# Optimization experiments

Hardware: AMD Instinct MI355X
Metric: run time of the kernel (lower is better)

Reference implementation:

```python
import jax, jax.numpy as jnp
import numpy as np

B = 65536            # batch of configurations
F = 32               # num_frames (joints)
DOF = 29             # controllable joints
# tree: chain 0..29, two mimic branches off frame 10; parent index always < child -> topo order = range(F)
PARENTS = [-1] + list(range(29)) + [10, 10]


def _np_rodrigues(w):
    th = np.linalg.norm(w)
    if th < 1e-12:
        return np.eye(3)
    k = w / th
    K = np.array([[0, -k[2], k[1]], [k[2], 0, -k[0]], [-k[1], k[0], 0]])
    return np.eye(3) + np.sin(th) * K + (1 - np.cos(th)) * (K @ K)


def setup_inputs() -> dict:
    key = jax.random.key(0)
    rng = np.random.default_rng(0)
    # joint types: 0 fixed, 1 revolute, 2 prismatic
    types = np.ones(F, dtype=np.int32)
    types[0] = 0
    types[15] = 2
    types[22] = 2
    # controllable = non-fixed, non-mimic (mimic dst = 30, 31)
    ctrl = np.array([i for i in range(F) if types[i] != 0 and i not in (30, 31)], dtype=np.int32)
    assert ctrl.shape[0] == DOF
    axes = rng.normal(size=(F, 3)).astype(np.float32)
    axes /= np.linalg.norm(axes, axis=-1, keepdims=True)
    origins = np.tile(np.eye(4, dtype=np.float32), (F, 1, 1))
    for i in range(F):
        origins[i, :3, :3] = _np_rodrigues(rng.normal(size=3) * 0.5)
        origins[i, :3, 3] = rng.normal(size=3) * 0.1
    joint_angles = jax.random.normal(key, (B, DOF), dtype=jnp.float32)
    return {
        "joint_angles": joint_angles,
        "all_axes": jnp.asarray(axes),
        "all_origins": jnp.asarray(origins),
        "mimic_multipliers": jnp.array([1.0, -1.0], dtype=jnp.float32),
        "mimic_offsets": jnp.array([0.1, -0.1], dtype=jnp.float32),
        "ctrlable_indices": jnp.asarray(ctrl),
        "mimic_src_indices": jnp.array([5, 6], dtype=jnp.int32),
        "mimic_dst_indices": jnp.array([30, 31], dtype=jnp.int32),
        "joint_types": jnp.asarray(types),
    }


def exp_map(w):
    # axis-angle (...,3) -> rotation (...,3,3), Rodrigues, eps-safe at w=0
    theta = jnp.sqrt(jnp.sum(w * w, axis=-1, keepdims=True) + 1e-18)  # (...,1)
    k = w / theta
    kx, ky, kz = k[..., 0], k[..., 1], k[..., 2]
    zero = jnp.zeros_like(kx)
    K = jnp.stack(
        [jnp.stack([zero, -kz, ky], -1),
         jnp.stack([kz, zero, -kx], -1),
         jnp.stack([-ky, kx, zero], -1)], -2)
    st = jnp.sin(theta)[..., None]
    ct = jnp.cos(theta)[..., None]
    return jnp.eye(3, dtype=w.dtype) + st * K + (1.0 - ct) * (K @ K)


def _fk(joint_angles, all_axes, all_origins, mimic_multipliers, mimic_offsets,
        ctrlable_indices, mimic_src_indices, mimic_dst_indices, joint_types):
    b = joint_angles.shape[0]
    # scatter controllable angles, then mimic gather/scatter
    all_angles = jnp.zeros((b, F), joint_angles.dtype).at[:, ctrlable_indices].set(joint_angles)
    mimic_vals = all_angles[:, mimic_src_indices] * mimic_multipliers + mimic_offsets
    all_angles = all_angles.at[:, mimic_dst_indices].set(mimic_vals)
    # per-frame local motion (B,F,4,4)
    w = all_axes[None, :, :] * all_angles[..., None]          # (B,F,3)
    R = exp_map(w)                                            # (B,F,3,3)
    R = jnp.where((joint_types == 1)[None, :, None, None], R, jnp.eye(3, dtype=w.dtype))
    t = jnp.where((joint_types == 2)[None, :, None], w, jnp.zeros((), w.dtype))
    top = jnp.concatenate([R, t[..., None]], axis=-1)         # (B,F,3,4)
    bottom = jnp.broadcast_to(jnp.array([0, 0, 0, 1], w.dtype), (b, F, 1, 4))
    motion = jnp.concatenate([top, bottom], axis=-2)          # (B,F,4,4)
    local = jnp.einsum('fij,bfjk->bfik', all_origins, motion)
    # sequential tree-structured compose (F is small & static -> unrolled)
    poses = []
    for i in range(F):
        p = PARENTS[i]
        li = local[:, i]
        poses.append(li if p < 0 else poses[p] @ li)
    return jnp.stack(poses, axis=1)                            # (B,F,4,4)


def reference(joint_angles, all_axes, all_origins, mimic_multipliers, mimic_offsets,
              ctrlable_indices, mimic_src_indices, mimic_dst_indices, joint_types):
    return _fk(joint_angles, all_axes, all_origins, mimic_multipliers, mimic_offsets,
               ctrlable_indices, mimic_src_indices, mimic_dst_indices, joint_types)
```

## Files before the change

kernel.cpp:

```cpp
#include <hip/hip_runtime.h>
#include <math.h>

#define BLOCK 256
#define NF 32
#define NDOF 29

__global__ __launch_bounds__(BLOCK) void fk_kernel(
    const float* __restrict__ ja,
    const float* __restrict__ axes,
    const float* __restrict__ origins,
    const float* __restrict__ mmul,
    const float* __restrict__ moff,
    const int*   __restrict__ ctrl,
    const int*   __restrict__ msrc,
    const int*   __restrict__ mdst,
    const int*   __restrict__ types,
    float*       __restrict__ out,
    int B)
{
    __shared__ float s_ax[NF][3];
    __shared__ float s_or[NF][12];
    __shared__ int   s_type[NF];
    __shared__ int   s_slot[NF];
    __shared__ float s_mult[NF];
    __shared__ float s_off[NF];
    __shared__ float s_ja[BLOCK * NDOF];

    const int tid = threadIdx.x;

    if (tid < NF) {
        const int f = tid;
        s_ax[f][0] = axes[f*3+0];
        s_ax[f][1] = axes[f*3+1];
        s_ax[f][2] = axes[f*3+2];
        #pragma unroll
        for (int r = 0; r < 3; ++r)
            #pragma unroll
            for (int c = 0; c < 4; ++c)
                s_or[f][r*4+c] = origins[f*16 + r*4 + c];
        s_type[f] = types[f];
        int slot = -1;
        for (int j = 0; j < NDOF; ++j) if (ctrl[j] == f) slot = j;
        float mu = 1.0f, of = 0.0f;
        for (int m = 0; m < 2; ++m) {
            if (mdst[m] == f) {
                const int sf = msrc[m];
                for (int j = 0; j < NDOF; ++j) if (ctrl[j] == sf) slot = j;
                mu = mmul[m]; of = moff[m];
            }
        }
        s_slot[f] = slot; s_mult[f] = mu; s_off[f] = of;
    }

    const long blk0 = (long)blockIdx.x * BLOCK;
    {
        const long base = blk0 * NDOF;
        const long lim  = (long)B * NDOF;
        for (int i = tid; i < BLOCK * NDOF; i += BLOCK) {
            const long g = base + i;
            s_ja[i] = (g < lim) ? ja[g] : 0.0f;
        }
    }
    __syncthreads();

    const long b = blk0 + tid;
    if (b >= B) return;

    float4* __restrict__ outp = (float4*)(out + b * 512);

    float Pr[9], Pt[3];
    float Qr[9], Qt[3];

    auto compute_local = [&](int f, float* Lr, float* Lt) {
        const int   slot = s_slot[f];
        const float a = (slot >= 0) ? fmaf(s_mult[f], s_ja[tid*NDOF + slot], s_off[f]) : 0.0f;
        const float wx = a * s_ax[f][0];
        const float wy = a * s_ax[f][1];
        const float wz = a * s_ax[f][2];
        const int ty = s_type[f];
        float R0,R1,R2,R3,R4,R5,R6,R7,R8;
        if (ty == 1) {
            const float t2 = wx*wx + wy*wy + wz*wz;
            const float th = sqrtf(t2 + 1e-18f);
            const float inv = 1.0f / th;
            const float kx = wx*inv, ky = wy*inv, kz = wz*inv;
            float s, c;
            __sincosf(th, &s, &c);
            const float v = 1.0f - c;
            R0 = fmaf(v*kx, kx, c);
            R1 = v*kx*ky - s*kz;
            R2 = v*kx*kz + s*ky;
            R3 = v*kx*ky + s*kz;
            R4 = fmaf(v*ky, ky, c);
            R5 = v*ky*kz - s*kx;
            R6 = v*kx*kz - s*ky;
            R7 = v*ky*kz + s*kx;
            R8 = fmaf(v*kz, kz, c);
        } else {
            R0=1.f;R1=0.f;R2=0.f;R3=0.f;R4=1.f;R5=0.f;R6=0.f;R7=0.f;R8=1.f;
        }
        float tx, tyv, tz;
        if (ty == 2) { tx = wx; tyv = wy; tz = wz; }
        else         { tx = 0.f; tyv = 0.f; tz = 0.f; }
        const float* O = s_or[f];
        #pragma unroll
        for (int r = 0; r < 3; ++r) {
            const float o0 = O[r*4+0], o1 = O[r*4+1], o2 = O[r*4+2], o3 = O[r*4+3];
            Lr[r*3+0] = o0*R0 + o1*R3 + o2*R6;
            Lr[r*3+1] = o0*R1 + o1*R4 + o2*R7;
            Lr[r*3+2] = o0*R2 + o1*R5 + o2*R8;
            Lt[r]     = o0*tx + o1*tyv + o2*tz + o3;
        }
    };

    auto store_pose = [&](int f, const float* r, const float* t) {
        outp[f*4+0] = make_float4(r[0], r[1], r[2], t[0]);
        outp[f*4+1] = make_float4(r[3], r[4], r[5], t[1]);
        outp[f*4+2] = make_float4(r[6], r[7], r[8], t[2]);
        outp[f*4+3] = make_float4(0.0f, 0.0f, 0.0f, 1.0f);
    };

    {
        float Lr[9], Lt[3];
        compute_local(0, Lr, Lt);
        #pragma unroll
        for (int i = 0; i < 9; ++i) Pr[i] = Lr[i];
        Pt[0] = Lt[0]; Pt[1] = Lt[1]; Pt[2] = Lt[2];
        store_pose(0, Pr, Pt);
    }

    #pragma unroll 1
    for (int f = 1; f <= 29; ++f) {
        float Lr[9], Lt[3], Nr[9], Nt[3];
        compute_local(f, Lr, Lt);
        #pragma unroll
        for (int r = 0; r < 3; ++r) {
            const float p0 = Pr[r*3+0], p1 = Pr[r*3+1], p2 = Pr[r*3+2];
            Nr[r*3+0] = p0*Lr[0] + p1*Lr[3] + p2*Lr[6];
            Nr[r*3+1] = p0*Lr[1] + p1*Lr[4] + p2*Lr[7];
            Nr[r*3+2] = p0*Lr[2] + p1*Lr[5] + p2*Lr[8];
            Nt[r]     = p0*Lt[0] + p1*Lt[1] + p2*Lt[2] + Pt[r];
        }
        #pragma unroll
        for (int i = 0; i < 9; ++i) Pr[i] = Nr[i];
        Pt[0] = Nt[0]; Pt[1] = Nt[1]; Pt[2] = Nt[2];
        store_pose(f, Pr, Pt);
        if (f == 10) {
            #pragma unroll
            for (int i = 0; i < 9; ++i) Qr[i] = Pr[i];
            Qt[0] = Pt[0]; Qt[1] = Pt[1]; Qt[2] = Pt[2];
        }
    }

    #pragma unroll 1
    for (int f = 30; f < 32; ++f) {
        float Lr[9], Lt[3], Nr[9], Nt[3];
        compute_local(f, Lr, Lt);
        #pragma unroll
        for (int r = 0; r < 3; ++r) {
            const float p0 = Qr[r*3+0], p1 = Qr[r*3+1], p2 = Qr[r*3+2];
            Nr[r*3+0] = p0*Lr[0] + p1*Lr[3] + p2*Lr[6];
            Nr[r*3+1] = p0*Lr[1] + p1*Lr[4] + p2*Lr[7];
            Nr[r*3+2] = p0*Lr[2] + p1*Lr[5] + p2*Lr[8];
            Nt[r]     = p0*Lt[0] + p1*Lt[1] + p2*Lt[2] + Qt[r];
        }
        store_pose(f, Nr, Nt);
    }
}

extern "C" void kernel_launch(void* const* d_in, const int* in_sizes, int n_in,
                              void* d_out, int out_size, void* d_ws, size_t ws_size,
                              hipStream_t stream) {
    const float* ja   = (const float*)d_in[0];
    const float* axes = (const float*)d_in[1];
    const float* orig = (const float*)d_in[2];
    const float* mmul = (const float*)d_in[3];
    const float* moff = (const float*)d_in[4];
    const int*   ctrl = (const int*)d_in[5];
    const int*   msrc = (const int*)d_in[6];
    const int*   mdst = (const int*)d_in[7];
    const int*   typs = (const int*)d_in[8];
    float* out = (float*)d_out;

    const int B = in_sizes[0] / NDOF;
    const int grid = (B + BLOCK - 1) / BLOCK;
    fk_kernel<<<grid, BLOCK, 0, stream>>>(ja, axes, orig, mmul, moff,
                                          ctrl, msrc, mdst, typs, out, B);
}
```

Measured before the change: 183.9 us.

## Stage output poses through LDS for coalesced stores and transpose angle buffer

Joint angles are now stored in shared memory transposed with a padded stride, so each thread's per-joint read avoids bank conflicts. Output poses are computed two frames at a time into a padded shared staging buffer and then written cooperatively, so consecutive threads store consecutive 128-byte chunks instead of each thread striding 2 KB apart. This is meant to make the dominant 128 MB output write coalesced. In exchange it adds 32 block-wide barriers, about 37 KB more LDS per block, which may lower occupancy, and a single loop that branches on frame index.

```diff
diff --git a/kernel.cpp b/kernel.cpp
--- a/kernel.cpp
+++ b/kernel.cpp
@@ -4,6 +4,8 @@
 #define BLOCK 256
 #define NF 32
 #define NDOF 29
+#define ANG_STRIDE 257
+#define OUT_STRIDE_F4 9
 
 __global__ __launch_bounds__(BLOCK) void fk_kernel(
     const float* __restrict__ ja,
@@ -24,7 +26,8 @@
     __shared__ int   s_slot[NF];
     __shared__ float s_mult[NF];
     __shared__ float s_off[NF];
-    __shared__ float s_ja[BLOCK * NDOF];
+    __shared__ float s_ang[NDOF * ANG_STRIDE];
+    __shared__ float4 s_out[BLOCK * OUT_STRIDE_F4];
 
     const int tid = threadIdx.x;
 
@@ -58,22 +61,20 @@
         const long lim  = (long)B * NDOF;
         for (int i = tid; i < BLOCK * NDOF; i += BLOCK) {
             const long g = base + i;
-            s_ja[i] = (g < lim) ? ja[g] : 0.0f;
+            const int slot = i % NDOF;
+            const int brel = i / NDOF;
+            s_ang[slot * ANG_STRIDE + brel] = (g < lim) ? ja[g] : 0.0f;
         }
     }
     __syncthreads();
-
-    const long b = blk0 + tid;
-    if (b >= B) return;
-
-    float4* __restrict__ outp = (float4*)(out + b * 512);
 
     float Pr[9], Pt[3];
     float Qr[9], Qt[3];
 
     auto compute_local = [&](int f, float* Lr, float* Lt) {
         const int   slot = s_slot[f];
-        const float a = (slot >= 0) ? fmaf(s_mult[f], s_ja[tid*NDOF + slot], s_off[f]) : 0.0f;
+        const float a = (slot >= 0)
+            ? fmaf(s_mult[f], s_ang[slot * ANG_STRIDE + tid], s_off[f]) : 0.0f;
         const float wx = a * s_ax[f][0];
         const float wy = a * s_ax[f][1];
         const float wz = a * s_ax[f][2];
@@ -113,58 +114,67 @@
         }
     };
 
-    auto store_pose = [&](int f, const float* r, const float* t) {
-        outp[f*4+0] = make_float4(r[0], r[1], r[2], t[0]);
-        outp[f*4+1] = make_float4(r[3], r[4], r[5], t[1]);
-        outp[f*4+2] = make_float4(r[6], r[7], r[8], t[2]);
-        outp[f*4+3] = make_float4(0.0f, 0.0f, 0.0f, 1.0f);
-    };
-
-    {
-        float Lr[9], Lt[3];
-        compute_local(0, Lr, Lt);
-        #pragma unroll
-        for (int i = 0; i < 9; ++i) Pr[i] = Lr[i];
-        Pt[0] = Lt[0]; Pt[1] = Lt[1]; Pt[2] = Lt[2];
-        store_pose(0, Pr, Pt);
-    }
+    float4* const out4 = (float4*)out;
 
     #pragma unroll 1
-    for (int f = 1; f <= 29; ++f) {
-        float Lr[9], Lt[3], Nr[9], Nt[3];
-        compute_local(f, Lr, Lt);
+    for (int c = 0; c < 16; ++c) {
+        const int f0 = 2 * c;
         #pragma unroll
-        for (int r = 0; r < 3; ++r) {
-            const float p0 = Pr[r*3+0], p1 = Pr[r*3+1], p2 = Pr[r*3+2];
-            Nr[r*3+0] = p0*Lr[0] + p1*Lr[3] + p2*Lr[6];
-            Nr[r*3+1] = p0*Lr[1] + p1*Lr[4] + p2*Lr[7];
-            Nr[r*3+2] = p0*Lr[2] + p1*Lr[5] + p2*Lr[8];
-            Nt[r]     = p0*Lt[0] + p1*Lt[1] + p2*Lt[2] + Pt[r];
+        for (int lf = 0; lf < 2; ++lf) {
+            const int f = f0 + lf;
+            float Lr[9], Lt[3];
+            compute_local(f, Lr, Lt);
+            float Wr[9], Wt[3];
+            if (f == 0) {
+                #pragma unroll
+                for (int i = 0; i < 9; ++i) Wr[i] = Lr[i];
+                Wt[0]=Lt[0]; Wt[1]=Lt[1]; Wt[2]=Lt[2];
+            } else if (f <= 29) {
+                #pragma unroll
+                for (int r = 0; r < 3; ++r) {
+                    const float p0 = Pr[r*3+0], p1 = Pr[r*3+1], p2 = Pr[r*3+2];
+                    Wr[r*3+0] = p0*Lr[0] + p1*Lr[3] + p2*Lr[6];
+                    Wr[r*3+1] = p0*Lr[1] + p1*Lr[4] + p2*Lr[7];
+                    Wr[r*3+2] = p0*Lr[2] + p1*Lr[5] + p2*Lr[8];
+                    Wt[r]     = p0*Lt[0] + p1*Lt[1] + p2*Lt[2] + Pt[r];
+                }
+            } else {
+                #pragma unroll
+                for (int r = 0; r < 3; ++r) {
+                    const float p0 = Qr[r*3+0], p1 = Qr[r*3+1], p2 = Qr[r*3+2];
+                    Wr[r*3+0] = p0*Lr[0] + p1*Lr[3] + p2*Lr[6];
+                    Wr[r*3+1] = p0*Lr[1] + p1*Lr[4] + p2*Lr[7];
+                    Wr[r*3+2] = p0*Lr[2] + p1*Lr[5] + p2*Lr[8];
+                    Wt[r]     = p0*Lt[0] + p1*Lt[1] + p2*Lt[2] + Qt[r];
+                }
+            }
+            if (f <= 29) {
+                #pragma unroll
+                for (int i = 0; i < 9; ++i) Pr[i] = Wr[i];
+                Pt[0]=Wt[0]; Pt[1]=Wt[1]; Pt[2]=Wt[2];
+                if (f == 10) {
+                    #pragma unroll
+                    for (int i = 0; i < 9; ++i) Qr[i] = Pr[i];
+                    Qt[0]=Pt[0]; Qt[1]=Pt[1]; Qt[2]=Pt[2];
+                }
+            }
+            float4* slot4 = &s_out[tid * OUT_STRIDE_F4 + lf * 4];
+            slot4[0] = make_float4(Wr[0], Wr[1], Wr[2], Wt[0]);
+            slot4[1] = make_float4(Wr[3], Wr[4], Wr[5], Wt[1]);
+            slot4[2] = make_float4(Wr[6], Wr[7], Wr[8], Wt[2]);
+            slot4[3] = make_float4(0.0f, 0.0f, 0.0f, 1.0f);
         }
+        __syncthreads();
         #pragma unroll
-        for (int i = 0; i < 9; ++i) Pr[i] = Nr[i];
-        Pt[0] = Nt[0]; Pt[1] = Nt[1]; Pt[2] = Nt[2];
-        store_pose(f, Pr, Pt);
-        if (f == 10) {
-            #pragma unroll
-            for (int i = 0; i < 9; ++i) Qr[i] = Pr[i];
-            Qt[0] = Pt[0]; Qt[1] = Pt[1]; Qt[2] = Pt[2];
+        for (int k = 0; k < 8; ++k) {
+            const int i = tid + k * BLOCK;
+            const int brel = i >> 3;
+            const int q    = i & 7;
+            const long bb  = blk0 + brel;
+            if (bb < (long)B)
+                out4[bb * 128 + f0 * 4 + q] = s_out[brel * OUT_STRIDE_F4 + q];
         }
-    }
-
-    #pragma unroll 1
-    for (int f = 30; f < 32; ++f) {
-        float Lr[9], Lt[3], Nr[9], Nt[3];
-        compute_local(f, Lr, Lt);
-        #pragma unroll
-        for (int r = 0; r < 3; ++r) {
-            const float p0 = Qr[r*3+0], p1 = Qr[r*3+1], p2 = Qr[r*3+2];
-            Nr[r*3+0] = p0*Lr[0] + p1*Lr[3] + p2*Lr[6];
-            Nr[r*3+1] = p0*Lr[1] + p1*Lr[4] + p2*Lr[7];
-            Nr[r*3+2] = p0*Lr[2] + p1*Lr[5] + p2*Lr[8];
-            Nt[r]     = p0*Lt[0] + p1*Lt[1] + p2*Lt[2] + Qt[r];
-        }
-        store_pose(f, Nr, Nt);
+        __syncthreads();
     }
 }
 
```

Result: faster. 170.6 us (-7.2%).

## Parallelize FK chain across lanes with pointer-jumping shuffle scan

Applied to the files above, without the earlier changes.

Assigns one thread per frame (32 lanes per batch element) instead of one thread per batch element, and composes the kinematic chain by pointer jumping over wavefront shuffles in five rounds. The aim is to replace the serial chain of 30 dependent matrix products with a log-depth parallel prefix and to make the output stores contiguous across lanes. The cost is redundant ctrl and mimic lookups per thread, more total multiply-adds, and many shuffles. Shared-memory staging of joint angles and constants is removed.

```diff
diff --git a/kernel.cpp b/kernel.cpp
--- a/kernel.cpp
+++ b/kernel.cpp
@@ -1,9 +1,9 @@
 #include <hip/hip_runtime.h>
 #include <math.h>
 
-#define BLOCK 256
 #define NF 32
 #define NDOF 29
+#define BLOCK 256
 
 __global__ __launch_bounds__(BLOCK) void fk_kernel(
     const float* __restrict__ ja,
@@ -18,154 +18,101 @@
     float*       __restrict__ out,
     int B)
 {
-    __shared__ float s_ax[NF][3];
-    __shared__ float s_or[NF][12];
-    __shared__ int   s_type[NF];
-    __shared__ int   s_slot[NF];
-    __shared__ float s_mult[NF];
-    __shared__ float s_off[NF];
-    __shared__ float s_ja[BLOCK * NDOF];
+    const int tid  = threadIdx.x;
+    const int lane = tid & 63;
+    const int f    = tid & 31;
+    const long b   = (long)blockIdx.x * (BLOCK / 32) + (tid >> 5);
+    if (b >= (long)B) return;
 
-    const int tid = threadIdx.x;
-
-    if (tid < NF) {
-        const int f = tid;
-        s_ax[f][0] = axes[f*3+0];
-        s_ax[f][1] = axes[f*3+1];
-        s_ax[f][2] = axes[f*3+2];
-        #pragma unroll
-        for (int r = 0; r < 3; ++r)
+    int slot = -1;
+    #pragma unroll
+    for (int j = 0; j < NDOF; ++j) if (ctrl[j] == f) slot = j;
+    float mu = 1.0f, of = 0.0f;
+    #pragma unroll
+    for (int m = 0; m < 2; ++m) {
+        if (mdst[m] == f) {
+            const int sf = msrc[m];
             #pragma unroll
-            for (int c = 0; c < 4; ++c)
-                s_or[f][r*4+c] = origins[f*16 + r*4 + c];
-        s_type[f] = types[f];
-        int slot = -1;
-        for (int j = 0; j < NDOF; ++j) if (ctrl[j] == f) slot = j;
-        float mu = 1.0f, of = 0.0f;
-        for (int m = 0; m < 2; ++m) {
-            if (mdst[m] == f) {
-                const int sf = msrc[m];
-                for (int j = 0; j < NDOF; ++j) if (ctrl[j] == sf) slot = j;
-                mu = mmul[m]; of = moff[m];
-            }
-        }
-        s_slot[f] = slot; s_mult[f] = mu; s_off[f] = of;
-    }
-
-    const long blk0 = (long)blockIdx.x * BLOCK;
-    {
-        const long base = blk0 * NDOF;
-        const long lim  = (long)B * NDOF;
-        for (int i = tid; i < BLOCK * NDOF; i += BLOCK) {
-            const long g = base + i;
-            s_ja[i] = (g < lim) ? ja[g] : 0.0f;
-        }
-    }
-    __syncthreads();
-
-    const long b = blk0 + tid;
-    if (b >= B) return;
-
-    float4* __restrict__ outp = (float4*)(out + b * 512);
-
-    float Pr[9], Pt[3];
-    float Qr[9], Qt[3];
-
-    auto compute_local = [&](int f, float* Lr, float* Lt) {
-        const int   slot = s_slot[f];
-        const float a = (slot >= 0) ? fmaf(s_mult[f], s_ja[tid*NDOF + slot], s_off[f]) : 0.0f;
-        const float wx = a * s_ax[f][0];
-        const float wy = a * s_ax[f][1];
-        const float wz = a * s_ax[f][2];
-        const int ty = s_type[f];
-        float R0,R1,R2,R3,R4,R5,R6,R7,R8;
-        if (ty == 1) {
-            const float t2 = wx*wx + wy*wy + wz*wz;
-            const float th = sqrtf(t2 + 1e-18f);
-            const float inv = 1.0f / th;
-            const float kx = wx*inv, ky = wy*inv, kz = wz*inv;
-            float s, c;
-            __sincosf(th, &s, &c);
-            const float v = 1.0f - c;
-            R0 = fmaf(v*kx, kx, c);
-            R1 = v*kx*ky - s*kz;
-            R2 = v*kx*kz + s*ky;
-            R3 = v*kx*ky + s*kz;
-            R4 = fmaf(v*ky, ky, c);
-            R5 = v*ky*kz - s*kx;
-            R6 = v*kx*kz - s*ky;
-            R7 = v*ky*kz + s*kx;
-            R8 = fmaf(v*kz, kz, c);
-        } else {
-            R0=1.f;R1=0.f;R2=0.f;R3=0.f;R4=1.f;R5=0.f;R6=0.f;R7=0.f;R8=1.f;
-        }
-        float tx, tyv, tz;
-        if (ty == 2) { tx = wx; tyv = wy; tz = wz; }
-        else         { tx = 0.f; tyv = 0.f; tz = 0.f; }
-        const float* O = s_or[f];
-        #pragma unroll
-        for (int r = 0; r < 3; ++r) {
-            const float o0 = O[r*4+0], o1 = O[r*4+1], o2 = O[r*4+2], o3 = O[r*4+3];
-            Lr[r*3+0] = o0*R0 + o1*R3 + o2*R6;
-            Lr[r*3+1] = o0*R1 + o1*R4 + o2*R7;
-            Lr[r*3+2] = o0*R2 + o1*R5 + o2*R8;
-            Lt[r]     = o0*tx + o1*tyv + o2*tz + o3;
-        }
-    };
-
-    auto store_pose = [&](int f, const float* r, const float* t) {
-        outp[f*4+0] = make_float4(r[0], r[1], r[2], t[0]);
-        outp[f*4+1] = make_float4(r[3], r[4], r[5], t[1]);
-        outp[f*4+2] = make_float4(r[6], r[7], r[8], t[2]);
-        outp[f*4+3] = make_float4(0.0f, 0.0f, 0.0f, 1.0f);
-    };
-
-    {
-        float Lr[9], Lt[3];
-        compute_local(0, Lr, Lt);
-        #pragma unroll
-        for (int i = 0; i < 9; ++i) Pr[i] = Lr[i];
-        Pt[0] = Lt[0]; Pt[1] = Lt[1]; Pt[2] = Lt[2];
-        store_pose(0, Pr, Pt);
-    }
-
-    #pragma unroll 1
-    for (int f = 1; f <= 29; ++f) {
-        float Lr[9], Lt[3], Nr[9], Nt[3];
-        compute_local(f, Lr, Lt);
-        #pragma unroll
-        for (int r = 0; r < 3; ++r) {
-            const float p0 = Pr[r*3+0], p1 = Pr[r*3+1], p2 = Pr[r*3+2];
-            Nr[r*3+0] = p0*Lr[0] + p1*Lr[3] + p2*Lr[6];
-            Nr[r*3+1] = p0*Lr[1] + p1*Lr[4] + p2*Lr[7];
-            Nr[r*3+2] = p0*Lr[2] + p1*Lr[5] + p2*Lr[8];
-            Nt[r]     = p0*Lt[0] + p1*Lt[1] + p2*Lt[2] + Pt[r];
-        }
-        #pragma unroll
-        for (int i = 0; i < 9; ++i) Pr[i] = Nr[i];
-        Pt[0] = Nt[0]; Pt[1] = Nt[1]; Pt[2] = Nt[2];
-        store_pose(f, Pr, Pt);
-        if (f == 10) {
-            #pragma unroll
-            for (int i = 0; i < 9; ++i) Qr[i] = Pr[i];
-            Qt[0] = Pt[0]; Qt[1] = Pt[1]; Qt[2] = Pt[2];
+            for (int j = 0; j < NDOF; ++j) if (ctrl[j] == sf) slot = j;
+            mu = mmul[m]; of = moff[m];
         }
     }
 
-    #pragma unroll 1
-    for (int f = 30; f < 32; ++f) {
-        float Lr[9], Lt[3], Nr[9], Nt[3];
-        compute_local(f, Lr, Lt);
+    const float a  = (slot >= 0) ? fmaf(mu, ja[b * NDOF + slot], of) : 0.0f;
+    const float wx = a * axes[f * 3 + 0];
+    const float wy = a * axes[f * 3 + 1];
+    const float wz = a * axes[f * 3 + 2];
+    const int   ty = types[f];
+
+    float R0,R1,R2,R3,R4,R5,R6,R7,R8;
+    if (ty == 1) {
+        const float t2 = wx*wx + wy*wy + wz*wz;
+        const float th = sqrtf(t2 + 1e-18f);
+        const float inv = 1.0f / th;
+        const float kx = wx*inv, ky = wy*inv, kz = wz*inv;
+        float s, c;
+        __sincosf(th, &s, &c);
+        const float v = 1.0f - c;
+        R0 = fmaf(v*kx, kx, c);
+        R1 = v*kx*ky - s*kz;
+        R2 = v*kx*kz + s*ky;
+        R3 = v*kx*ky + s*kz;
+        R4 = fmaf(v*ky, ky, c);
+        R5 = v*ky*kz - s*kx;
+        R6 = v*kx*kz - s*ky;
+        R7 = v*ky*kz + s*kx;
+        R8 = fmaf(v*kz, kz, c);
+    } else {
+        R0=1.f;R1=0.f;R2=0.f;R3=0.f;R4=1.f;R5=0.f;R6=0.f;R7=0.f;R8=1.f;
+    }
+    const float tx  = (ty == 2) ? wx : 0.0f;
+    const float tyv = (ty == 2) ? wy : 0.0f;
+    const float tz  = (ty == 2) ? wz : 0.0f;
+
+    float M[12];
+    {
+        const float4* O4 = (const float4*)origins;
         #pragma unroll
         for (int r = 0; r < 3; ++r) {
-            const float p0 = Qr[r*3+0], p1 = Qr[r*3+1], p2 = Qr[r*3+2];
-            Nr[r*3+0] = p0*Lr[0] + p1*Lr[3] + p2*Lr[6];
-            Nr[r*3+1] = p0*Lr[1] + p1*Lr[4] + p2*Lr[7];
-            Nr[r*3+2] = p0*Lr[2] + p1*Lr[5] + p2*Lr[8];
-            Nt[r]     = p0*Lt[0] + p1*Lt[1] + p2*Lt[2] + Qt[r];
+            const float4 O = O4[f * 4 + r];
+            M[r*4+0] = O.x*R0 + O.y*R3 + O.z*R6;
+            M[r*4+1] = O.x*R1 + O.y*R4 + O.z*R7;
+            M[r*4+2] = O.x*R2 + O.y*R5 + O.z*R8;
+            M[r*4+3] = O.x*tx + O.y*tyv + O.z*tz + O.w;
         }
-        store_pose(f, Nr, Nt);
     }
+
+    int ptr = (f == 0) ? -1 : ((f >= 30) ? 10 : (f - 1));
+    const int half = lane & 32;
+
+    #pragma unroll
+    for (int it = 0; it < 5; ++it) {
+        const int src = half | (ptr & 31);
+        float P[12];
+        #pragma unroll
+        for (int i = 0; i < 12; ++i) P[i] = __shfl(M[i], src, 64);
+        const int pptr = __shfl(ptr, src, 64);
+        if (ptr >= 0) {
+            float N[12];
+            #pragma unroll
+            for (int r = 0; r < 3; ++r) {
+                const float p0 = P[r*4+0], p1 = P[r*4+1], p2 = P[r*4+2], p3 = P[r*4+3];
+                N[r*4+0] = p0*M[0] + p1*M[4] + p2*M[8];
+                N[r*4+1] = p0*M[1] + p1*M[5] + p2*M[9];
+                N[r*4+2] = p0*M[2] + p1*M[6] + p2*M[10];
+                N[r*4+3] = p0*M[3] + p1*M[7] + p2*M[11] + p3;
+            }
+            #pragma unroll
+            for (int i = 0; i < 12; ++i) M[i] = N[i];
+            ptr = pptr;
+        }
+    }
+
+    float4* o = (float4*)(out + b * 512 + f * 16);
+    o[0] = make_float4(M[0], M[1], M[2],  M[3]);
+    o[1] = make_float4(M[4], M[5], M[6],  M[7]);
+    o[2] = make_float4(M[8], M[9], M[10], M[11]);
+    o[3] = make_float4(0.0f, 0.0f, 0.0f,  1.0f);
 }
 
 extern "C" void kernel_launch(void* const* d_in, const int* in_sizes, int n_in,
@@ -183,7 +130,8 @@
     float* out = (float*)d_out;
 
     const int B = in_sizes[0] / NDOF;
-    const int grid = (B + BLOCK - 1) / BLOCK;
+    const int batches_per_block = BLOCK / 32;
+    const int grid = (B + batches_per_block - 1) / batches_per_block;
     fk_kernel<<<grid, BLOCK, 0, stream>>>(ja, axes, orig, mmul, moff,
                                           ctrl, msrc, mdst, typs, out, B);
 }
```

Result: faster. 180.2 us (-2.0%).
